# Kernel tuning notes

Measured on AMD Instinct MI355X. Metric: run time of the kernel, lower is better.

## Reference

```python
import jax, jax.numpy as jnp
import numpy as np

B, S = 128, 4096            # batch, num memory slots
W_NUM = 10000               # word_num (vocab)
CONT, FEAT, LSTM = 256, 256, 256
AH, CH = 128, 128           # actor/critic hidden dims
EPS = 1e-8


def _lin(key, out_d, in_d):
    k1, k2 = jax.random.split(key)
    s = 1.0 / np.sqrt(in_d)
    W = jax.random.uniform(k1, (out_d, in_d), jnp.float32, -s, s)
    b = jax.random.uniform(k2, (out_d,), jnp.float32, -s, s)
    return W, b


def setup_inputs() -> dict:
    key = jax.random.key(0)
    ks = jax.random.split(key, 18)
    d = {}
    d['x'] = jax.random.normal(ks[0], (B, W_NUM), jnp.float32)
    d['feat'] = jax.random.normal(ks[1], (B, S, FEAT), jnp.float32)
    d['h_tm1'] = jax.random.normal(ks[2], (B, LSTM), jnp.float32)
    d['c_tm1'] = jax.random.normal(ks[3], (B, LSTM), jnp.float32)
    d['W_x2cont'], d['b_x2cont'] = _lin(ks[4], CONT, W_NUM)
    d['W_h2cont'], d['b_h2cont'] = _lin(ks[5], CONT, LSTM)
    d['W_cont2key'], d['b_cont2key'] = _lin(ks[6], FEAT, CONT)
    d['W_cont2strength'], d['b_cont2strength'] = _lin(ks[7], 1, CONT)
    d['W_att_gates'], d['b_att_gates'] = _lin(ks[8], 1, FEAT + LSTM + CONT)
    d['W_ih'], d['b_ih'] = _lin(ks[9], 4 * LSTM, CONT + FEAT)
    d['W_hh'], d['b_hh'] = _lin(ks[10], 4 * LSTM, LSTM)
    d['W_actor_hid'], d['b_actor_hid'] = _lin(ks[11], AH, LSTM)
    d['W_critic_hid'], d['b_critic_hid'] = _lin(ks[12], CH, LSTM)
    d['W_actor'], d['b_actor'] = _lin(ks[13], W_NUM, AH)
    d['W_critic'], d['b_critic'] = _lin(ks[14], 1, CH)
    return d


def reference(x, feat, h_tm1, c_tm1,
              W_x2cont, b_x2cont, W_h2cont, b_h2cont,
              W_cont2key, b_cont2key, W_cont2strength, b_cont2strength,
              W_att_gates, b_att_gates, W_ih, b_ih, W_hh, b_hh,
              W_actor_hid, b_actor_hid, W_critic_hid, b_critic_hid,
              W_actor, b_actor, W_critic, b_critic):
    lin = lambda v, W, b: v @ W.T + b
    # controller
    x_cont = lin(x, W_x2cont, b_x2cont)                      # [B, CONT]
    h_cont = lin(h_tm1, W_h2cont, b_h2cont)                  # [B, CONT]
    control = jax.nn.relu(x_cont + h_cont)
    key_v = jnp.tanh(lin(control, W_cont2key, b_cont2key))   # [B, FEAT]
    strength = jax.nn.relu(lin(control, W_cont2strength, b_cont2strength)) + 1.0  # [B,1]
    # NTM-style content addressing: sharpened cosine similarity -> softmax over slots
    feat_n = jnp.linalg.norm(feat, axis=-1)                  # [B, S]
    key_n = jnp.linalg.norm(key_v, axis=-1, keepdims=True)   # [B, 1]
    sim = jnp.einsum('bsd,bd->bs', feat, key_v) / (feat_n * key_n + EPS)
    alpha = jax.nn.softmax(strength * sim, axis=-1)          # [B, S]
    cand_att_vec = jnp.einsum('bs,bsd->bd', alpha, feat)     # [B, FEAT]
    # attention gate
    gate_in = jnp.concatenate([cand_att_vec, h_tm1, x_cont], axis=1)  # [B, FEAT+LSTM+CONT]
    gates_att = jax.nn.sigmoid(lin(gate_in, W_att_gates, b_att_gates))
    att_vec = cand_att_vec * gates_att
    # LSTM cell (PyTorch gate order: i, f, g, o)
    inp_lstm = jnp.concatenate([att_vec, x_cont], axis=1)    # [B, FEAT+CONT]
    g = lin(inp_lstm, W_ih, b_ih) + lin(h_tm1, W_hh, b_hh)
    i, f, gg, o = jnp.split(g, 4, axis=1)
    c = jax.nn.sigmoid(f) * c_tm1 + jax.nn.sigmoid(i) * jnp.tanh(gg)
    h = jax.nn.sigmoid(o) * jnp.tanh(c)
    # heads
    action_logit = lin(jax.nn.relu(lin(h, W_actor_hid, b_actor_hid)), W_actor, b_actor)
    value = lin(jax.nn.relu(lin(h, W_critic_hid, b_critic_hid)), W_critic, b_critic)
    return (action_logit, value, h, c)
```

## Files before the change

### kernel.cpp

```cpp
#include <hip/hip_runtime.h>
#include <cmath>


#define B_ 128
#define S_ 4096
#define WN 10000
#define CD 256

__global__ __launch_bounds__(256) void k1_xcont(
    const float* __restrict__ x, const float* __restrict__ Wx,
    float* __restrict__ part) {
  const int nt = blockIdx.x;
  const int ks = blockIdx.y;
  const int t = threadIdx.x;
  __shared__ float4 xs[128][16];
  __shared__ float4 wsW[16][16];
  const int o0 = nt * 16;
  const int og = t & 3;
  const int bg = t >> 2;
  const int bgx = bg & 7;
  float acc[2][4] = {{0.f, 0.f, 0.f, 0.f}, {0.f, 0.f, 0.f, 0.f}};
  for (int sub = 0; sub < 4; ++sub) {
    const int k0 = ks * 256 + sub * 64;
    for (int q = t; q < 2048; q += 256) {
      const int row = q >> 4, c4 = q & 15;
      const int k = k0 + c4 * 4;
      float4 v = make_float4(0.f, 0.f, 0.f, 0.f);
      if (k < WN) v = *(const float4*)(x + (size_t)row * WN + k);
      xs[row][c4 ^ (row & 7)] = v;
    }
    {
      const int row = t >> 4, c4 = t & 15;
      const int k = k0 + c4 * 4;
      float4 v = make_float4(0.f, 0.f, 0.f, 0.f);
      if (k < WN) v = *(const float4*)(Wx + (size_t)(o0 + row) * WN + k);
      wsW[row][c4 ^ (row & 7)] = v;
    }
    __syncthreads();
#pragma unroll
    for (int c4 = 0; c4 < 16; ++c4) {
      float4 wv[4];
#pragma unroll
      for (int i = 0; i < 4; ++i) wv[i] = wsW[og * 4 + i][c4 ^ ((og * 4 + i) & 7)];
#pragma unroll
      for (int j = 0; j < 2; ++j) {
        const float4 xv = xs[bg + j * 64][c4 ^ bgx];
#pragma unroll
        for (int i = 0; i < 4; ++i)
          acc[j][i] += xv.x * wv[i].x + xv.y * wv[i].y + xv.z * wv[i].z + xv.w * wv[i].w;
      }
    }
    __syncthreads();
  }
#pragma unroll
  for (int j = 0; j < 2; ++j) {
    const int bb = bg + j * 64;
#pragma unroll
    for (int i = 0; i < 4; ++i)
      part[(size_t)ks * 32768 + bb * 256 + o0 + og * 4 + i] = acc[j][i];
  }
}

__global__ __launch_bounds__(256) void k2_controller(
    const float* __restrict__ part, const float* __restrict__ bx,
    const float* __restrict__ h_tm1, const float* __restrict__ Wh,
    const float* __restrict__ bh, const float* __restrict__ Wk,
    const float* __restrict__ bk, const float* __restrict__ Ws,
    const float* __restrict__ bs, float* __restrict__ x_cont,
    float* __restrict__ key_v, float* __restrict__ strength,
    float* __restrict__ key_n) {
  const int b = blockIdx.x, t = threadIdx.x;
  __shared__ float hs[256], cs[256];
  __shared__ float r1[4], r2[4];
  hs[t] = h_tm1[b * 256 + t];
  float xc = bx[t];
  for (int ks = 0; ks < 40; ++ks) xc += part[(size_t)ks * 32768 + b * 256 + t];
  x_cont[b * 256 + t] = xc;
  __syncthreads();
  float hc = bh[t];
  {
    const float* w = Wh + (size_t)t * 256;
    for (int k = 0; k < 256; k += 4) {
      float4 wv = *(const float4*)(w + k);
      hc += hs[k] * wv.x + hs[k + 1] * wv.y + hs[k + 2] * wv.z + hs[k + 3] * wv.w;
    }
  }
  const float ctl = fmaxf(xc + hc, 0.f);
  cs[t] = ctl;
  __syncthreads();
  float kvv = bk[t];
  {
    const float* w = Wk + (size_t)t * 256;
    for (int k = 0; k < 256; k += 4) {
      float4 wv = *(const float4*)(w + k);
      kvv += cs[k] * wv.x + cs[k + 1] * wv.y + cs[k + 2] * wv.z + cs[k + 3] * wv.w;
    }
  }
  kvv = tanhf(kvv);
  key_v[b * 256 + t] = kvv;
  float v1 = kvv * kvv;
  float v2 = ctl * Ws[t];
  for (int off = 32; off; off >>= 1) {
    v1 += __shfl_xor(v1, off);
    v2 += __shfl_xor(v2, off);
  }
  const int w_ = t >> 6, lane = t & 63;
  if (lane == 0) { r1[w_] = v1; r2[w_] = v2; }
  __syncthreads();
  if (t == 0) {
    const float n2 = r1[0] + r1[1] + r1[2] + r1[3];
    const float sd = r2[0] + r2[1] + r2[2] + r2[3];
    key_n[b] = sqrtf(n2);
    strength[b] = fmaxf(sd + bs[0], 0.f) + 1.f;
  }
}

__device__ __forceinline__ float dpp_add16(float x) {
  int t;
  t = __builtin_amdgcn_update_dpp(0, __float_as_int(x), 0x121, 0xf, 0xf, true);
  x += __int_as_float(t);
  t = __builtin_amdgcn_update_dpp(0, __float_as_int(x), 0x122, 0xf, 0xf, true);
  x += __int_as_float(t);
  t = __builtin_amdgcn_update_dpp(0, __float_as_int(x), 0x124, 0xf, 0xf, true);
  x += __int_as_float(t);
  t = __builtin_amdgcn_update_dpp(0, __float_as_int(x), 0x128, 0xf, 0xf, true);
  x += __int_as_float(t);
  return x;
}

__global__ __launch_bounds__(256) void k3_attn(
    const float* __restrict__ feat, const float* __restrict__ key_v,
    const float* __restrict__ strength, const float* __restrict__ key_n,
    float* __restrict__ att_part) {
  const int ss = blockIdx.x;
  const int b = blockIdx.y;
  const int t = threadIdx.x;
  const int w = t >> 6, lane = t & 63;
  const int g = lane >> 4;
  const int l = lane & 15;

  __shared__ __align__(16) float tile[2][16][256];
  __shared__ float wo[4][256];
  __shared__ float wl[4];

  const float str = strength[b];
  const float kn = key_n[b];
  float4 kf[4];
#pragma unroll
  for (int p = 0; p < 4; ++p)
    kf[p] = *(const float4*)(key_v + b * 256 + p * 64 + l * 4);

  const float* fbase = feat + ((size_t)b * S_ + (size_t)ss * 512) * 256;

#define STAGE(nt, buf)                                                        \
  {                                                                           \
    _Pragma("unroll") for (int j = 0; j < 4; ++j) {                           \
      const int row_ = w * 4 + j;                                             \
      const float* gp_ = fbase + ((size_t)(nt)*16 + row_) * 256 + lane * 4;   \
      __builtin_amdgcn_global_load_lds(                                       \
          (const __attribute__((address_space(1))) void*)gp_,                 \
          (__attribute__((address_space(3))) void*)&tile[buf][row_][0], 16,   \
          0, 18);                                                             \
    }                                                                         \
  }

  float4 o[4];
#pragma unroll
  for (int p = 0; p < 4; ++p) o[p] = make_float4(0.f, 0.f, 0.f, 0.f);
  float lsum = 0.f;

#define COMPUTE(buf)                                                          \
  {                                                                           \
    const int row_ = w * 4 + g;                                               \
    const float* rp_ = &tile[buf][row_][l * 4];                               \
    const float4 f0 = *(const float4*)(rp_);                                  \
    const float4 f1 = *(const float4*)(rp_ + 64);                             \
    const float4 f2 = *(const float4*)(rp_ + 128);                            \
    const float4 f3 = *(const float4*)(rp_ + 192);                            \
    float dp0 = f0.x * kf[0].x + f0.y * kf[0].y + f0.z * kf[0].z + f0.w * kf[0].w; \
    float dp1 = f1.x * kf[1].x + f1.y * kf[1].y + f1.z * kf[1].z + f1.w * kf[1].w; \
    float dp2 = f2.x * kf[2].x + f2.y * kf[2].y + f2.z * kf[2].z + f2.w * kf[2].w; \
    float dp3 = f3.x * kf[3].x + f3.y * kf[3].y + f3.z * kf[3].z + f3.w * kf[3].w; \
    float nn0 = f0.x * f0.x + f0.y * f0.y + f0.z * f0.z + f0.w * f0.w;        \
    float nn1 = f1.x * f1.x + f1.y * f1.y + f1.z * f1.z + f1.w * f1.w;        \
    float nn2 = f2.x * f2.x + f2.y * f2.y + f2.z * f2.z + f2.w * f2.w;        \
    float nn3 = f3.x * f3.x + f3.y * f3.y + f3.z * f3.z + f3.w * f3.w;        \
    float d_ = (dp0 + dp1) + (dp2 + dp3);                                     \
    float n2_ = (nn0 + nn1) + (nn2 + nn3);                                    \
    d_ = dpp_add16(d_);                                                       \
    n2_ = dpp_add16(n2_);                                                     \
    const float sc_ = str * d_ / (sqrtf(n2_) * kn + 1e-8f);                   \
    const float a_ = __expf(sc_ - str);                                       \
    lsum += a_;                                                               \
    o[0].x += a_ * f0.x; o[0].y += a_ * f0.y; o[0].z += a_ * f0.z; o[0].w += a_ * f0.w; \
    o[1].x += a_ * f1.x; o[1].y += a_ * f1.y; o[1].z += a_ * f1.z; o[1].w += a_ * f1.w; \
    o[2].x += a_ * f2.x; o[2].y += a_ * f2.y; o[2].z += a_ * f2.z; o[2].w += a_ * f2.w; \
    o[3].x += a_ * f3.x; o[3].y += a_ * f3.y; o[3].z += a_ * f3.z; o[3].w += a_ * f3.w; \
  }

  STAGE(0, 0);
  STAGE(1, 1);
#pragma unroll 1
  for (int nt = 0; nt < 30; ++nt) {
    asm volatile("s_waitcnt vmcnt(4)" ::: "memory");
    COMPUTE(nt & 1);
    STAGE(nt + 2, nt & 1);
  }
  asm volatile("s_waitcnt vmcnt(4)" ::: "memory");
  COMPUTE(0);
  asm volatile("s_waitcnt vmcnt(0)" ::: "memory");
  COMPUTE(1);
#undef STAGE
#undef COMPUTE

#pragma unroll
  for (int off = 16; off <= 32; off <<= 1) {
    lsum += __shfl_xor(lsum, off);
#pragma unroll
    for (int p = 0; p < 4; ++p) {
      o[p].x += __shfl_xor(o[p].x, off);
      o[p].y += __shfl_xor(o[p].y, off);
      o[p].z += __shfl_xor(o[p].z, off);
      o[p].w += __shfl_xor(o[p].w, off);
    }
  }
  if (g == 0) {
#pragma unroll
    for (int p = 0; p < 4; ++p) *(float4*)&wo[w][p * 64 + l * 4] = o[p];
    if (l == 0) wl[w] = lsum;
  }
  __syncthreads();
  const float od = wo[0][t] + wo[1][t] + wo[2][t] + wo[3][t];
  float* apo = att_part + (size_t)(b * 8 + ss) * 264;
  if (t == 0) apo[0] = wl[0] + wl[1] + wl[2] + wl[3];
  apo[4 + t] = od;
}

__global__ __launch_bounds__(256) void k4a_gate(
    const float* __restrict__ att_part, const float* __restrict__ h_tm1,
    const float* __restrict__ x_cont, const float* __restrict__ Wg,
    const float* __restrict__ bg_, float* __restrict__ inp_cat) {
  const int b = blockIdx.x, t = threadIdx.x;
  const float* ap = att_part + (size_t)b * 8 * 264;
  float lg = 0.f, od = 0.f;
#pragma unroll
  for (int ss = 0; ss < 8; ++ss) {
    lg += ap[ss * 264];
    od += ap[ss * 264 + 4 + t];
  }
  const float cand = od / lg;
  const float hv = h_tm1[b * 256 + t];
  const float xc = x_cont[b * 256 + t];
  float v = cand * Wg[t] + hv * Wg[256 + t] + xc * Wg[512 + t];
  for (int off = 32; off; off >>= 1) v += __shfl_xor(v, off);
  __shared__ float rr[4];
  __shared__ float gsh;
  const int w_ = t >> 6, lane = t & 63;
  if (lane == 0) rr[w_] = v;
  __syncthreads();
  if (t == 0) {
    const float s = rr[0] + rr[1] + rr[2] + rr[3] + bg_[0];
    gsh = 1.f / (1.f + expf(-s));
  }
  __syncthreads();
  inp_cat[b * 768 + t] = cand * gsh;
  inp_cat[b * 768 + 256 + t] = xc;
  inp_cat[b * 768 + 512 + t] = hv;
}

__global__ __launch_bounds__(256) void k4b_lstm(
    const float* __restrict__ inp_cat, const float* __restrict__ Wih,
    const float* __restrict__ bih, const float* __restrict__ Whh,
    const float* __restrict__ bhh, const float* __restrict__ c_tm1,
    float* __restrict__ h_out, float* __restrict__ c_out) {
  const int j0 = blockIdx.x * 2;
  const int t = threadIdx.x;
  __shared__ float inp_s[128][132];
  __shared__ float w_s[8][132];
  const int b = t >> 1, half = t & 1;
  float acc[4] = {0.f, 0.f, 0.f, 0.f};
  for (int kc = 0; kc < 6; ++kc) {
    const int kbase = kc * 128;
    for (int q = t; q < 4096; q += 256) {
      const int row = q >> 5, c4 = q & 31;
      *(float4*)&inp_s[row][c4 * 4] =
          *(const float4*)(inp_cat + (size_t)row * 768 + kbase + c4 * 4);
    }
    {
      const int row = t >> 5, c4 = t & 31;
      const int gate = row & 3;
      const int j = j0 + (row >> 2);
      const int og = gate * 256 + j;
      const int kg = kbase + c4 * 4;
      float4 v;
      if (kg < 512) v = *(const float4*)(Wih + (size_t)og * 512 + kg);
      else          v = *(const float4*)(Whh + (size_t)og * 256 + (kg - 512));
      *(float4*)&w_s[row][c4 * 4] = v;
    }
    __syncthreads();
    for (int k = 0; k < 128; k += 4) {
      const float4 iv = *(const float4*)&inp_s[b][k];
#pragma unroll
      for (int g = 0; g < 4; ++g) {
        const float4 wv = *(const float4*)&w_s[half * 4 + g][k];
        acc[g] += iv.x * wv.x + iv.y * wv.y + iv.z * wv.z + iv.w * wv.w;
      }
    }
    __syncthreads();
  }
  const int j = j0 + half;
  const float gi = acc[0] + bih[j] + bhh[j];
  const float gf = acc[1] + bih[256 + j] + bhh[256 + j];
  const float gg = acc[2] + bih[512 + j] + bhh[512 + j];
  const float go = acc[3] + bih[768 + j] + bhh[768 + j];
  const float ct = c_tm1[b * 256 + j];
  const float i_ = 1.f / (1.f + expf(-gi));
  const float f_ = 1.f / (1.f + expf(-gf));
  const float g_ = tanhf(gg);
  const float o_ = 1.f / (1.f + expf(-go));
  const float c = f_ * ct + i_ * g_;
  const float h = o_ * tanhf(c);
  h_out[b * 256 + j] = h;
  c_out[b * 256 + j] = c;
}

__global__ __launch_bounds__(256) void k5_hid(
    const float* __restrict__ h_in, const float* __restrict__ Wah,
    const float* __restrict__ bah, const float* __restrict__ Wch,
    const float* __restrict__ bch, float* __restrict__ hidA,
    float* __restrict__ hidC) {
  const int b = blockIdx.x, t = threadIdx.x;
  __shared__ float hs[256];
  hs[t] = h_in[b * 256 + t];
  __syncthreads();
  const float* W = (t < 128) ? (Wah + (size_t)t * 256) : (Wch + (size_t)(t - 128) * 256);
  float s = (t < 128) ? bah[t] : bch[t - 128];
  for (int k = 0; k < 256; k += 4) {
    const float4 w = *(const float4*)(W + k);
    s += hs[k] * w.x + hs[k + 1] * w.y + hs[k + 2] * w.z + hs[k + 3] * w.w;
  }
  s = fmaxf(s, 0.f);
  if (t < 128) hidA[b * 128 + t] = s;
  else         hidC[b * 128 + (t - 128)] = s;
}

__global__ __launch_bounds__(256) void k6_heads(
    const float* __restrict__ hidA, const float* __restrict__ hidC,
    const float* __restrict__ Wa, const float* __restrict__ ba,
    const float* __restrict__ Wc, const float* __restrict__ bc,
    float* __restrict__ logits, float* __restrict__ value) {
  const int t = threadIdx.x;
  const int bx = blockIdx.x, by = blockIdx.y;
  if (bx == 157) {
    if (by == 0 && t < 128) {
      const float* hc = hidC + (size_t)t * 128;
      float s = bc[0];
      for (int k = 0; k < 128; k += 4) {
        const float4 w = *(const float4*)(Wc + k);
        s += hc[k] * w.x + hc[k + 1] * w.y + hc[k + 2] * w.z + hc[k + 3] * w.w;
      }
      value[t] = s;
    }
    return;
  }
  const int o0 = bx * 64;
  const int b0 = by * 32;
  __shared__ float4 ha[32][32];
  __shared__ float4 wa[64][32];
  for (int q = t; q < 1024; q += 256) {
    const int row = q >> 5, c4 = q & 31;
    ha[row][c4 ^ ((row >> 2) & 7)] =
        *(const float4*)(hidA + (size_t)(b0 + row) * 128 + c4 * 4);
  }
  for (int q = t; q < 2048; q += 256) {
    const int row = q >> 5, c4 = q & 31;
    const int o = o0 + row;
    float4 v = make_float4(0.f, 0.f, 0.f, 0.f);
    if (o < WN) v = *(const float4*)(Wa + (size_t)o * 128 + c4 * 4);
    wa[row][c4 ^ ((row >> 2) & 7)] = v;
  }
  __syncthreads();
  const int og = t & 15, bq = t >> 4;
  float acc[2][4];
#pragma unroll
  for (int r = 0; r < 2; ++r)
#pragma unroll
    for (int i = 0; i < 4; ++i) acc[r][i] = 0.f;
#pragma unroll 4
  for (int c4 = 0; c4 < 32; ++c4) {
    float4 wv[4];
#pragma unroll
    for (int i = 0; i < 4; ++i) wv[i] = wa[og * 4 + i][c4 ^ (og & 7)];
#pragma unroll
    for (int r = 0; r < 2; ++r) {
      const int row = bq * 2 + r;
      const float4 hv = ha[row][c4 ^ ((row >> 2) & 7)];
#pragma unroll
      for (int i = 0; i < 4; ++i)
        acc[r][i] += hv.x * wv[i].x + hv.y * wv[i].y + hv.z * wv[i].z + hv.w * wv[i].w;
    }
  }
  const int obase = o0 + og * 4;
#pragma unroll
  for (int r = 0; r < 2; ++r) {
    const int bb = b0 + bq * 2 + r;
    if (obase + 3 < WN) {
      const float4 bias = *(const float4*)(ba + obase);
      float4 res;
      res.x = acc[r][0] + bias.x;
      res.y = acc[r][1] + bias.y;
      res.z = acc[r][2] + bias.z;
      res.w = acc[r][3] + bias.w;
      *(float4*)(logits + (size_t)bb * WN + obase) = res;
    } else {
      for (int i = 0; i < 4; ++i)
        if (obase + i < WN) logits[(size_t)bb * WN + obase + i] = acc[r][i] + ba[obase + i];
    }
  }
}

extern "C" void kernel_launch(void* const* d_in, const int* in_sizes, int n_in,
                              void* d_out, int out_size, void* d_ws, size_t ws_size,
                              hipStream_t stream) {
  const float* x     = (const float*)d_in[0];
  const float* feat  = (const float*)d_in[1];
  const float* h_tm1 = (const float*)d_in[2];
  const float* c_tm1 = (const float*)d_in[3];
  const float* Wx2c  = (const float*)d_in[4];
  const float* bx2c  = (const float*)d_in[5];
  const float* Wh2c  = (const float*)d_in[6];
  const float* bh2c  = (const float*)d_in[7];
  const float* Wc2k  = (const float*)d_in[8];
  const float* bc2k  = (const float*)d_in[9];
  const float* Wc2s  = (const float*)d_in[10];
  const float* bc2s  = (const float*)d_in[11];
  const float* Wag   = (const float*)d_in[12];
  const float* bag   = (const float*)d_in[13];
  const float* Wih   = (const float*)d_in[14];
  const float* bih   = (const float*)d_in[15];
  const float* Whh   = (const float*)d_in[16];
  const float* bhh   = (const float*)d_in[17];
  const float* Wah   = (const float*)d_in[18];
  const float* bah   = (const float*)d_in[19];
  const float* Wch   = (const float*)d_in[20];
  const float* bch   = (const float*)d_in[21];
  const float* Wa    = (const float*)d_in[22];
  const float* ba    = (const float*)d_in[23];
  const float* Wc    = (const float*)d_in[24];
  const float* bc    = (const float*)d_in[25];

  float* out    = (float*)d_out;
  float* logits = out;
  float* value  = out + 1280000;
  float* h_out  = out + 1280128;
  float* c_out  = out + 1312896;

  float* wsf      = (float*)d_ws;
  float* part     = wsf;
  float* x_cont   = part + 1310720;
  float* key_v    = x_cont + 32768;
  float* strength = key_v + 32768;
  float* key_n    = strength + 128;
  float* att_part = key_n + 128;
  float* inp_cat  = att_part + 270336;
  float* hidA     = inp_cat + 98304;
  float* hidC     = hidA + 16384;

  k1_xcont<<<dim3(16, 40), 256, 0, stream>>>(x, Wx2c, part);
  k2_controller<<<128, 256, 0, stream>>>(part, bx2c, h_tm1, Wh2c, bh2c,
                                         Wc2k, bc2k, Wc2s, bc2s,
                                         x_cont, key_v, strength, key_n);
  k3_attn<<<dim3(8, 128), 256, 0, stream>>>(feat, key_v, strength, key_n, att_part);
  k4a_gate<<<128, 256, 0, stream>>>(att_part, h_tm1, x_cont, Wag, bag, inp_cat);
  k4b_lstm<<<128, 256, 0, stream>>>(inp_cat, Wih, bih, Whh, bhh, c_tm1, h_out, c_out);
  k5_hid<<<128, 256, 0, stream>>>(h_out, Wah, bah, Wch, bch, hidA, hidC);
  k6_heads<<<dim3(158, 4), 256, 0, stream>>>(hidA, hidC, Wa, ba, Wc, bc, logits, value);
}
```

Baseline: 240.6 us.

## Fuse attention gate, LSTM cell and hidden heads into one per-batch kernel

Merges the gate, LSTM and hidden-layer kernels into a single kernel with one block per batch row. The concatenated LSTM input and the new h now stay in shared memory, which removes two launches and the inp_cat round trip through global memory. In exchange, every block streams the full W_ih and W_hh matrices on its own, with each thread reading its own weight row. That drops the cross-batch weight reuse the old tiled LSTM kernel had and makes the per-thread weight reads poorly coalesced.

```diff
diff --git a/kernel.cpp b/kernel.cpp
--- a/kernel.cpp
+++ b/kernel.cpp
@@ -236,11 +236,22 @@
   apo[4 + t] = od;
 }
 
-__global__ __launch_bounds__(256) void k4a_gate(
+__global__ __launch_bounds__(256) void km_fused(
     const float* __restrict__ att_part, const float* __restrict__ h_tm1,
-    const float* __restrict__ x_cont, const float* __restrict__ Wg,
-    const float* __restrict__ bg_, float* __restrict__ inp_cat) {
+    const float* __restrict__ c_tm1, const float* __restrict__ x_cont,
+    const float* __restrict__ Wg, const float* __restrict__ bg_,
+    const float* __restrict__ Wih, const float* __restrict__ bih,
+    const float* __restrict__ Whh, const float* __restrict__ bhh,
+    const float* __restrict__ Wah, const float* __restrict__ bah,
+    const float* __restrict__ Wch, const float* __restrict__ bch,
+    float* __restrict__ h_out, float* __restrict__ c_out,
+    float* __restrict__ hidA, float* __restrict__ hidC) {
   const int b = blockIdx.x, t = threadIdx.x;
+  __shared__ float inp[768];
+  __shared__ float hsh[256];
+  __shared__ float rr[4];
+  __shared__ float gsh;
+
   const float* ap = att_part + (size_t)b * 8 * 264;
   float lg = 0.f, od = 0.f;
 #pragma unroll
@@ -253,8 +264,6 @@
   const float xc = x_cont[b * 256 + t];
   float v = cand * Wg[t] + hv * Wg[256 + t] + xc * Wg[512 + t];
   for (int off = 32; off; off >>= 1) v += __shfl_xor(v, off);
-  __shared__ float rr[4];
-  __shared__ float gsh;
   const int w_ = t >> 6, lane = t & 63;
   if (lane == 0) rr[w_] = v;
   __syncthreads();
@@ -263,81 +272,65 @@
     gsh = 1.f / (1.f + expf(-s));
   }
   __syncthreads();
-  inp_cat[b * 768 + t] = cand * gsh;
-  inp_cat[b * 768 + 256 + t] = xc;
-  inp_cat[b * 768 + 512 + t] = hv;
-}
-
-__global__ __launch_bounds__(256) void k4b_lstm(
-    const float* __restrict__ inp_cat, const float* __restrict__ Wih,
-    const float* __restrict__ bih, const float* __restrict__ Whh,
-    const float* __restrict__ bhh, const float* __restrict__ c_tm1,
-    float* __restrict__ h_out, float* __restrict__ c_out) {
-  const int j0 = blockIdx.x * 2;
-  const int t = threadIdx.x;
-  __shared__ float inp_s[128][132];
-  __shared__ float w_s[8][132];
-  const int b = t >> 1, half = t & 1;
-  float acc[4] = {0.f, 0.f, 0.f, 0.f};
-  for (int kc = 0; kc < 6; ++kc) {
-    const int kbase = kc * 128;
-    for (int q = t; q < 4096; q += 256) {
-      const int row = q >> 5, c4 = q & 31;
-      *(float4*)&inp_s[row][c4 * 4] =
-          *(const float4*)(inp_cat + (size_t)row * 768 + kbase + c4 * 4);
-    }
-    {
-      const int row = t >> 5, c4 = t & 31;
-      const int gate = row & 3;
-      const int j = j0 + (row >> 2);
-      const int og = gate * 256 + j;
-      const int kg = kbase + c4 * 4;
-      float4 v;
-      if (kg < 512) v = *(const float4*)(Wih + (size_t)og * 512 + kg);
-      else          v = *(const float4*)(Whh + (size_t)og * 256 + (kg - 512));
-      *(float4*)&w_s[row][c4 * 4] = v;
-    }
-    __syncthreads();
-    for (int k = 0; k < 128; k += 4) {
-      const float4 iv = *(const float4*)&inp_s[b][k];
-#pragma unroll
-      for (int g = 0; g < 4; ++g) {
-        const float4 wv = *(const float4*)&w_s[half * 4 + g][k];
-        acc[g] += iv.x * wv.x + iv.y * wv.y + iv.z * wv.z + iv.w * wv.w;
-      }
-    }
-    __syncthreads();
-  }
-  const int j = j0 + half;
-  const float gi = acc[0] + bih[j] + bhh[j];
-  const float gf = acc[1] + bih[256 + j] + bhh[256 + j];
-  const float gg = acc[2] + bih[512 + j] + bhh[512 + j];
-  const float go = acc[3] + bih[768 + j] + bhh[768 + j];
-  const float ct = c_tm1[b * 256 + j];
-  const float i_ = 1.f / (1.f + expf(-gi));
-  const float f_ = 1.f / (1.f + expf(-gf));
-  const float g_ = tanhf(gg);
-  const float o_ = 1.f / (1.f + expf(-go));
+  inp[t] = cand * gsh;
+  inp[256 + t] = xc;
+  inp[512 + t] = hv;
+  __syncthreads();
+
+  float a0 = bih[t] + bhh[t];
+  float a1 = bih[256 + t] + bhh[256 + t];
+  float a2 = bih[512 + t] + bhh[512 + t];
+  float a3 = bih[768 + t] + bhh[768 + t];
+  const float* wi0 = Wih + (size_t)t * 512;
+  const float* wi1 = Wih + (size_t)(256 + t) * 512;
+  const float* wi2 = Wih + (size_t)(512 + t) * 512;
+  const float* wi3 = Wih + (size_t)(768 + t) * 512;
+#pragma unroll 4
+  for (int k = 0; k < 512; k += 4) {
+    const float4 iv = *(const float4*)&inp[k];
+    const float4 w0 = *(const float4*)(wi0 + k);
+    const float4 w1 = *(const float4*)(wi1 + k);
+    const float4 w2 = *(const float4*)(wi2 + k);
+    const float4 w3 = *(const float4*)(wi3 + k);
+    a0 += iv.x * w0.x + iv.y * w0.y + iv.z * w0.z + iv.w * w0.w;
+    a1 += iv.x * w1.x + iv.y * w1.y + iv.z * w1.z + iv.w * w1.w;
+    a2 += iv.x * w2.x + iv.y * w2.y + iv.z * w2.z + iv.w * w2.w;
+    a3 += iv.x * w3.x + iv.y * w3.y + iv.z * w3.z + iv.w * w3.w;
+  }
+  const float* wh0 = Whh + (size_t)t * 256;
+  const float* wh1 = Whh + (size_t)(256 + t) * 256;
+  const float* wh2 = Whh + (size_t)(512 + t) * 256;
+  const float* wh3 = Whh + (size_t)(768 + t) * 256;
+#pragma unroll 4
+  for (int k = 0; k < 256; k += 4) {
+    const float4 iv = *(const float4*)&inp[512 + k];
+    const float4 w0 = *(const float4*)(wh0 + k);
+    const float4 w1 = *(const float4*)(wh1 + k);
+    const float4 w2 = *(const float4*)(wh2 + k);
+    const float4 w3 = *(const float4*)(wh3 + k);
+    a0 += iv.x * w0.x + iv.y * w0.y + iv.z * w0.z + iv.w * w0.w;
+    a1 += iv.x * w1.x + iv.y * w1.y + iv.z * w1.z + iv.w * w1.w;
+    a2 += iv.x * w2.x + iv.y * w2.y + iv.z * w2.z + iv.w * w2.w;
+    a3 += iv.x * w3.x + iv.y * w3.y + iv.z * w3.z + iv.w * w3.w;
+  }
+  const float ct = c_tm1[b * 256 + t];
+  const float i_ = 1.f / (1.f + expf(-a0));
+  const float f_ = 1.f / (1.f + expf(-a1));
+  const float g_ = tanhf(a2);
+  const float o_ = 1.f / (1.f + expf(-a3));
   const float c = f_ * ct + i_ * g_;
   const float h = o_ * tanhf(c);
-  h_out[b * 256 + j] = h;
-  c_out[b * 256 + j] = c;
-}
-
-__global__ __launch_bounds__(256) void k5_hid(
-    const float* __restrict__ h_in, const float* __restrict__ Wah,
-    const float* __restrict__ bah, const float* __restrict__ Wch,
-    const float* __restrict__ bch, float* __restrict__ hidA,
-    float* __restrict__ hidC) {
-  const int b = blockIdx.x, t = threadIdx.x;
-  __shared__ float hs[256];
-  hs[t] = h_in[b * 256 + t];
-  __syncthreads();
+  h_out[b * 256 + t] = h;
+  c_out[b * 256 + t] = c;
+  hsh[t] = h;
+  __syncthreads();
+
   const float* W = (t < 128) ? (Wah + (size_t)t * 256) : (Wch + (size_t)(t - 128) * 256);
   float s = (t < 128) ? bah[t] : bch[t - 128];
+#pragma unroll 4
   for (int k = 0; k < 256; k += 4) {
-    const float4 w = *(const float4*)(W + k);
-    s += hs[k] * w.x + hs[k + 1] * w.y + hs[k + 2] * w.z + hs[k + 3] * w.w;
+    const float4 wv = *(const float4*)(W + k);
+    s += hsh[k] * wv.x + hsh[k + 1] * wv.y + hsh[k + 2] * wv.z + hsh[k + 3] * wv.w;
   }
   s = fmaxf(s, 0.f);
   if (t < 128) hidA[b * 128 + t] = s;
@@ -462,8 +455,7 @@
   float* strength = key_v + 32768;
   float* key_n    = strength + 128;
   float* att_part = key_n + 128;
-  float* inp_cat  = att_part + 270336;
-  float* hidA     = inp_cat + 98304;
+  float* hidA     = att_part + 270336;
   float* hidC     = hidA + 16384;
 
   k1_xcont<<<dim3(16, 40), 256, 0, stream>>>(x, Wx2c, part);
@@ -471,8 +463,9 @@
                                          Wc2k, bc2k, Wc2s, bc2s,
                                          x_cont, key_v, strength, key_n);
   k3_attn<<<dim3(8, 128), 256, 0, stream>>>(feat, key_v, strength, key_n, att_part);
-  k4a_gate<<<128, 256, 0, stream>>>(att_part, h_tm1, x_cont, Wag, bag, inp_cat);
-  k4b_lstm<<<128, 256, 0, stream>>>(inp_cat, Wih, bih, Whh, bhh, c_tm1, h_out, c_out);
-  k5_hid<<<128, 256, 0, stream>>>(h_out, Wah, bah, Wch, bch, hidA, hidC);
+  km_fused<<<128, 256, 0, stream>>>(att_part, h_tm1, c_tm1, x_cont,
+                                    Wag, bag, Wih, bih, Whh, bhh,
+                                    Wah, bah, Wch, bch,
+                                    h_out, c_out, hidA, hidC);
   k6_heads<<<dim3(158, 4), 256, 0, stream>>>(hidA, hidC, Wa, ba, Wc, bc, logits, value);
 }
```

Result: slower. 297.7 us (+23.7%).
